# Optimization experiments

Hardware: AMD Instinct MI355X
Metric: run time of the kernel (lower is better)

The kernel has to match this reference:

```python
import jax, jax.numpy as jnp
import numpy as np

H = 16      # num_heads
D = 64      # hidden_size per head
IN = 1024   # input_size = H*D
B, S = 4, 2048

def setup_inputs() -> dict:
    key = jax.random.key(0)
    ks = jax.random.split(key, 5)
    scale = 1.0 / np.sqrt(IN)
    return {
        "x": jax.random.normal(ks[0], (B, S, IN), dtype=jnp.float32),
        "Wq": jax.random.normal(ks[1], (IN, H * D), dtype=jnp.float32) * scale,
        "bq": jnp.zeros((H * D,), dtype=jnp.float32),
        "Wk": jax.random.normal(ks[2], (IN, H * D), dtype=jnp.float32) * scale,
        "bk": jnp.zeros((H * D,), dtype=jnp.float32),
        "Wv": jax.random.normal(ks[3], (IN, H * D), dtype=jnp.float32) * scale,
        "bv": jnp.zeros((H * D,), dtype=jnp.float32),
        "Wo": jax.random.normal(ks[4], (H * D, IN), dtype=jnp.float32) * scale,
        "bo": jnp.zeros((IN,), dtype=jnp.float32),
    }

def reference(x, Wq, bq, Wk, bk, Wv, bv, Wo, bo):
    b, s, _ = x.shape
    # projections -> [b, h, s, d]
    def split_heads(t):
        return t.reshape(b, s, H, D).transpose(0, 2, 1, 3)
    q = split_heads(x @ Wq + bq)
    k = split_heads(x @ Wk + bk)
    v = split_heads(x @ Wv + bv)
    scores = jnp.einsum('bhqd,bhkd->bhqk', q, k) / jnp.sqrt(jnp.float32(D))
    probs = jax.nn.softmax(scores, axis=-1)            # [b,h,s,s]
    attn = jnp.einsum('bhqk,bhkd->bhqd', probs, v)     # [b,h,s,d]
    attn = attn.transpose(0, 2, 1, 3).reshape(b, s, H * D)
    out = attn @ Wo + bo
    return out, jnp.mean(probs, axis=1)
```

## Files before the change

### kernel.cpp

```cpp
#include <hip/hip_runtime.h>

typedef __attribute__((ext_vector_type(8))) short s8v;
typedef __attribute__((ext_vector_type(4))) short s4v;
typedef __attribute__((ext_vector_type(4))) float f4v;

#define DEV __device__ __forceinline__

DEV short b16(float f) {
  unsigned u = __builtin_bit_cast(unsigned, f);
  u = (u + 0x7fffu + ((u >> 16) & 1u)) >> 16;
  return (short)u;
}

DEV unsigned pk2(float a, float b) {
#if __has_builtin(__builtin_amdgcn_cvt_pk_bf16_f32)
  auto p = __builtin_amdgcn_cvt_pk_bf16_f32(a, b);
  return __builtin_bit_cast(unsigned, p);
#else
  return (unsigned)(unsigned short)b16(a) | ((unsigned)(unsigned short)b16(b) << 16);
#endif
}

DEV float fexp2(float x) {
#if __has_builtin(__builtin_amdgcn_exp2f)
  return __builtin_amdgcn_exp2f(x);
#else
  return exp2f(x);
#endif
}

DEV void gl_lds16(const short* g, short* l) {
  __builtin_amdgcn_global_load_lds((const __attribute__((address_space(1))) void*)g,
                                   (__attribute__((address_space(3))) void*)l, 16, 0, 0);
}

__global__ __launch_bounds__(256) void cast_f32_bf16(const float* __restrict__ in,
                                                     short* __restrict__ out, int n4) {
  int i = blockIdx.x * 256 + threadIdx.x;
  if (i >= n4) return;
  float4 v = ((const float4*)in)[i];
  s4v o; o.x = b16(v.x); o.y = b16(v.y); o.z = b16(v.z); o.w = b16(v.w);
  ((s4v*)out)[i] = o;
}

__global__ __launch_bounds__(256) void wtrans(const float* __restrict__ W, short* __restrict__ Wt) {
  int id = blockIdx.x * 256 + threadIdx.x;
  int k8 = id >> 10;
  int n  = id & 1023;
  s8v o;
#pragma unroll
  for (int j = 0; j < 8; ++j) o[j] = b16(W[(k8 * 8 + j) * 1024 + n]);
  *(s8v*)&Wt[n * 1024 + k8 * 8] = o;
}

template <bool OUT_BF16>
__global__ __launch_bounds__(256) void gemm128(const short* __restrict__ A,
                                               const short* __restrict__ Bt,
                                               const float* __restrict__ bias,
                                               void* __restrict__ Cout, float scale) {
  __shared__ short As[128 * 64];
  __shared__ short Bs[128 * 64];
  const int tid = threadIdx.x;
  const int w = tid >> 6, lane = tid & 63, quad = lane >> 4, l15 = lane & 15;
  const int wm = w >> 1, wn = w & 1;
  const int m0 = blockIdx.y * 128, n0 = blockIdx.x * 128;
  const int lr = lane >> 3, lc = (lane & 7) * 8;
  f4v acc[4][4] = {};
  for (int k0 = 0; k0 < 1024; k0 += 64) {
#pragma unroll
    for (int i = 0; i < 4; ++i) {
      int c = i * 4 + w;
      int r = c * 8 + lr;
      gl_lds16(&A[(m0 + r) * 1024 + k0 + lc], &As[c * 512]);
      gl_lds16(&Bt[(n0 + r) * 1024 + k0 + lc], &Bs[c * 512]);
    }
    __syncthreads();
#pragma unroll
    for (int kk = 0; kk < 2; ++kk) {
      s8v af[4], bf[4];
#pragma unroll
      for (int mt = 0; mt < 4; ++mt) af[mt] = *(const s8v*)&As[(wm * 64 + mt * 16 + l15) * 64 + kk * 32 + quad * 8];
#pragma unroll
      for (int nt = 0; nt < 4; ++nt) bf[nt] = *(const s8v*)&Bs[(wn * 64 + nt * 16 + l15) * 64 + kk * 32 + quad * 8];
#pragma unroll
      for (int mt = 0; mt < 4; ++mt)
#pragma unroll
        for (int nt = 0; nt < 4; ++nt)
          acc[mt][nt] = __builtin_amdgcn_mfma_f32_16x16x32_bf16(af[mt], bf[nt], acc[mt][nt], 0, 0, 0);
    }
    __syncthreads();
  }
#pragma unroll
  for (int nt = 0; nt < 4; ++nt) {
    const int col = n0 + wn * 64 + nt * 16 + l15;
    const float bcol = bias[col];
#pragma unroll
    for (int mt = 0; mt < 4; ++mt)
#pragma unroll
      for (int r = 0; r < 4; ++r) {
        const int row = m0 + wm * 64 + mt * 16 + quad * 4 + r;
        float v = (acc[mt][nt][r] + bcol) * scale;
        if (OUT_BF16) ((short*)Cout)[row * 1024 + col] = b16(v);
        else          ((float*)Cout)[row * 1024 + col] = v;
      }
  }
}

__global__ __launch_bounds__(256) void vtrans(const short* __restrict__ V, short* __restrict__ Vt) {
  __shared__ short T[128][72];
  const int st = blockIdx.x, h = blockIdx.y, b = blockIdx.z;
  const int tid = threadIdx.x;
#pragma unroll
  for (int i = 0; i < 4; ++i) {
    int c = tid + i * 256;
    int r = c >> 3, c8 = (c & 7) * 8;
    *(s8v*)&T[r][c8] = *(const s8v*)&V[((b * 2048 + st * 128 + r) * 16 + h) * 64 + c8];
  }
  __syncthreads();
#pragma unroll
  for (int i = 0; i < 4; ++i) {
    int id = tid + i * 256;
    int d = id & 63, s8 = id >> 6;
    s8v o;
#pragma unroll
    for (int j = 0; j < 8; ++j) o[j] = T[s8 * 8 + j][d];
    *(s8v*)&Vt[((b * 16 + h) * 64 + d) * 2048 + st * 128 + s8 * 8] = o;
  }
}

__global__ __launch_bounds__(256, 3) void attn_ctx(const short* __restrict__ Q, const short* __restrict__ K,
                                                   const short* __restrict__ Vt,
                                                   float* __restrict__ rbuf, short* __restrict__ ctx) {
  __shared__ __align__(16) char smem[50432];
  short* Ks = (short*)smem;
  short* Vs = (short*)(smem + 16384);
  short* Ps = (short*)(smem + 32768);
  short* Qs = Ps;
  float* l_part = (float*)(smem + 49152);
  float* l_s    = (float*)(smem + 50176);
  const int q64 = blockIdx.x, h = blockIdx.y, b = blockIdx.z;
  const int tid = threadIdx.x, w = tid >> 6, lane = tid & 63, quad = lane >> 4, l15 = lane & 15;
  const int bh = b * 16 + h, q0 = q64 * 64;

#pragma unroll
  for (int i = 0; i < 2; ++i) {
    int c = tid + i * 256;
    int r = c >> 3, cc = c & 7;
    *(s8v*)&Qs[r * 64 + (((cc ^ (r & 7))) << 3)] =
        *(const s8v*)&Q[((b * 2048 + q0 + r) * 16 + h) * 64 + cc * 8];
  }
  __syncthreads();
  s8v qf[4][2];
#pragma unroll
  for (int nt = 0; nt < 4; ++nt) {
    int r = nt * 16 + l15;
    qf[nt][0] = *(const s8v*)&Qs[r * 64 + ((quad ^ (r & 7)) << 3)];
    qf[nt][1] = *(const s8v*)&Qs[r * 64 + (((4 + quad) ^ (r & 7)) << 3)];
  }
  const short* kbase = &K[((long)(b * 2048) * 16 + h) * 64];
  const short* vbase = &Vt[(long)(bh * 64) * 2048];
  const int krow = w * 8 + (lane >> 3);
  const short* ksrc = kbase + krow * 1024 + (((lane & 7) ^ (lane >> 3)) << 3);
  const int vrow = w * 4 + (lane >> 4);
  const short* vsrc = vbase + vrow * 2048 + (((lane & 15) ^ vrow) << 3);
  f4v o[4] = {};
  float l_acc[4] = {0.f, 0.f, 0.f, 0.f};

  for (int kt = 0; kt < 16; ++kt) {
    __syncthreads();
#pragma unroll
    for (int i = 0; i < 4; ++i) {
      gl_lds16(ksrc + kt * 131072 + i * 32768, &Ks[(i * 4 + w) * 512]);
      gl_lds16(vsrc + kt * 128 + i * 32768, &Vs[(i * 4 + w) * 512]);
    }
    __syncthreads();
#pragma unroll
    for (int mt = 0; mt < 2; ++mt) {
      int kr = w * 32 + mt * 16 + l15;
      s8v a0 = *(const s8v*)&Ks[kr * 64 + ((quad ^ (kr & 7)) << 3)];
      s8v a1 = *(const s8v*)&Ks[kr * 64 + (((4 + quad) ^ (kr & 7)) << 3)];
#pragma unroll
      for (int nt = 0; nt < 4; ++nt) {
        f4v st = {};
        st = __builtin_amdgcn_mfma_f32_16x16x32_bf16(a0, qf[nt][0], st, 0, 0, 0);
        st = __builtin_amdgcn_mfma_f32_16x16x32_bf16(a1, qf[nt][1], st, 0, 0, 0);
        float e0 = fexp2(st[0]), e1 = fexp2(st[1]);
        float e2 = fexp2(st[2]), e3 = fexp2(st[3]);
        l_acc[nt] += (e0 + e1) + (e2 + e3);
        uint2 pp; pp.x = pk2(e0, e1); pp.y = pk2(e2, e3);
        int q = nt * 16 + l15;
        int chunk = (w * 4 + mt * 2 + (quad >> 1)) ^ l15;
        *(uint2*)&Ps[q * 128 + (chunk << 3) + (quad & 1) * 4] = pp;
      }
    }
    __syncthreads();
#pragma unroll
    for (int kk = 0; kk < 4; ++kk) {
      int qr = w * 16 + l15;
      s8v a = *(const s8v*)&Ps[qr * 128 + (((kk * 4 + quad) ^ (qr & 15)) << 3)];
#pragma unroll
      for (int dt = 0; dt < 4; ++dt) {
        int d = dt * 16 + l15;
        s8v vb = *(const s8v*)&Vs[d * 128 + (((kk * 4 + quad) ^ (d & 15)) << 3)];
        o[dt] = __builtin_amdgcn_mfma_f32_16x16x32_bf16(a, vb, o[dt], 0, 0, 0);
      }
    }
  }

#pragma unroll
  for (int nt = 0; nt < 4; ++nt) {
    float v = l_acc[nt];
    v += __shfl_xor(v, 16, 64);
    v += __shfl_xor(v, 32, 64);
    if (quad == 0) l_part[w * 64 + nt * 16 + l15] = v;
  }
  __syncthreads();
  if (tid < 64) {
    float s = l_part[tid] + l_part[64 + tid] + l_part[128 + tid] + l_part[192 + tid];
    float rv = 1.0f / s;
    l_s[tid] = rv;
    rbuf[bh * 2048 + q0 + tid] = rv;
  }
  __syncthreads();
  float rvq[4];
#pragma unroll
  for (int r = 0; r < 4; ++r) rvq[r] = l_s[w * 16 + quad * 4 + r];
#pragma unroll
  for (int dt = 0; dt < 4; ++dt)
#pragma unroll
    for (int r = 0; r < 4; ++r) {
      int sq = q0 + w * 16 + quad * 4 + r;
      ctx[((b * 2048 + sq) * 16 + h) * 64 + dt * 16 + l15] = b16(o[dt][r] * rvq[r]);
    }
}

__global__ __launch_bounds__(256) void mean_probs(const short* __restrict__ Q, const short* __restrict__ K,
                                                  const float* __restrict__ rbuf, float* __restrict__ outm) {
  __shared__ __align__(16) short Qs[8192];
  __shared__ __align__(16) short Ks[8192];
  __shared__ float r_s[128];
  const int k128 = blockIdx.x, q128 = blockIdx.y, b = blockIdx.z;
  const int tid = threadIdx.x, w = tid >> 6, lane = tid & 63, quad = lane >> 4, l15 = lane & 15;
  f4v mn[2][8] = {};
  const int mrow = w * 8 + (lane >> 3);
  const int mck8 = ((lane & 7) ^ (lane >> 3)) << 3;
  const short* qsrc = Q + ((long)(b * 2048 + q128 * 128 + mrow) * 16) * 64 + mck8;
  const short* ksrc = K + ((long)(b * 2048 + k128 * 128 + mrow) * 16) * 64 + mck8;
  for (int h = 0; h < 16; ++h) {
    __syncthreads();
#pragma unroll
    for (int i = 0; i < 4; ++i) {
      gl_lds16(qsrc + h * 64 + i * 32768, &Qs[(i * 4 + w) * 512]);
      gl_lds16(ksrc + h * 64 + i * 32768, &Ks[(i * 4 + w) * 512]);
    }
    if (tid < 128) r_s[tid] = rbuf[(b * 16 + h) * 2048 + q128 * 128 + tid] * 0.0625f;
    __syncthreads();
    s8v aq[2][2];
#pragma unroll
    for (int qt = 0; qt < 2; ++qt) {
      int r = w * 32 + qt * 16 + l15;
      aq[qt][0] = *(const s8v*)&Qs[r * 64 + ((quad ^ (r & 7)) << 3)];
      aq[qt][1] = *(const s8v*)&Qs[r * 64 + (((4 + quad) ^ (r & 7)) << 3)];
    }
    float rr[2][4];
#pragma unroll
    for (int qt = 0; qt < 2; ++qt)
#pragma unroll
      for (int r = 0; r < 4; ++r) rr[qt][r] = r_s[w * 32 + qt * 16 + quad * 4 + r];
#pragma unroll
    for (int ktile = 0; ktile < 8; ++ktile) {
      int kr = ktile * 16 + l15;
      s8v b0 = *(const s8v*)&Ks[kr * 64 + ((quad ^ (kr & 7)) << 3)];
      s8v b1 = *(const s8v*)&Ks[kr * 64 + (((4 + quad) ^ (kr & 7)) << 3)];
#pragma unroll
      for (int qt = 0; qt < 2; ++qt) {
        f4v sc = {};
        sc = __builtin_amdgcn_mfma_f32_16x16x32_bf16(aq[qt][0], b0, sc, 0, 0, 0);
        sc = __builtin_amdgcn_mfma_f32_16x16x32_bf16(aq[qt][1], b1, sc, 0, 0, 0);
#pragma unroll
        for (int r = 0; r < 4; ++r)
          mn[qt][ktile][r] += fexp2(sc[r]) * rr[qt][r];
      }
    }
  }
#pragma unroll
  for (int qt = 0; qt < 2; ++qt)
#pragma unroll
    for (int ktile = 0; ktile < 8; ++ktile)
#pragma unroll
      for (int r = 0; r < 4; ++r) {
        long qrow = q128 * 128 + w * 32 + qt * 16 + quad * 4 + r;
        outm[((long)b * 2048 + qrow) * 2048 + k128 * 128 + ktile * 16 + l15] = mn[qt][ktile][r];
      }
}

extern "C" void kernel_launch(void* const* d_in, const int* in_sizes, int n_in,
                              void* d_out, int out_size, void* d_ws, size_t ws_size,
                              hipStream_t stream) {
  (void)in_sizes; (void)n_in; (void)out_size; (void)ws_size;
  const float* x  = (const float*)d_in[0];
  const float* Wq = (const float*)d_in[1];
  const float* bq = (const float*)d_in[2];
  const float* Wk = (const float*)d_in[3];
  const float* bk = (const float*)d_in[4];
  const float* Wv = (const float*)d_in[5];
  const float* bv = (const float*)d_in[6];
  const float* Wo = (const float*)d_in[7];
  const float* bo = (const float*)d_in[8];
  float* out  = (float*)d_out;
  float* outm = out + 8388608;

  char* ws = (char*)d_ws;
  short* xb  = (short*)(ws);
  short* Wqt = (short*)(ws + 16777216);
  short* Wkt = (short*)(ws + 18874368);
  short* Wvt = (short*)(ws + 20971520);
  short* Wot = (short*)(ws + 23068672);
  short* Qb  = (short*)(ws + 25165824);
  short* Kb  = (short*)(ws + 41943040);
  short* Vb  = (short*)(ws + 58720256);
  short* Vt  = (short*)(ws + 75497472);
  float* rbuf = (float*)Vb;
  short* ctx = xb;

  const float C2 = 0.18033688011112042f;

  cast_f32_bf16<<<8192, 256, 0, stream>>>(x, xb, 2097152);
  wtrans<<<512, 256, 0, stream>>>(Wq, Wqt);
  wtrans<<<512, 256, 0, stream>>>(Wk, Wkt);
  wtrans<<<512, 256, 0, stream>>>(Wv, Wvt);
  wtrans<<<512, 256, 0, stream>>>(Wo, Wot);
  dim3 gg(8, 64);
  gemm128<true><<<gg, 256, 0, stream>>>(xb, Wqt, bq, Qb, C2);
  gemm128<true><<<gg, 256, 0, stream>>>(xb, Wkt, bk, Kb, 1.0f);
  gemm128<true><<<gg, 256, 0, stream>>>(xb, Wvt, bv, Vb, 1.0f);
  vtrans<<<dim3(16, 16, 4), 256, 0, stream>>>(Vb, Vt);
  attn_ctx<<<dim3(32, 16, 4), 256, 0, stream>>>(Qb, Kb, Vt, rbuf, ctx);
  mean_probs<<<dim3(16, 16, 4), 256, 0, stream>>>(Qb, Kb, rbuf, outm);
  gemm128<false><<<gg, 256, 0, stream>>>(ctx, Wot, bo, out, 1.0f);
}
```

Baseline: 445.4 us.

## Software-pipeline K/V and Q/K loads in attention and mean-probs kernels

The attention kernel now issues the next tile's K loads during the PV phase and the next V loads after it, with manual vmcnt waits and barriers in place of full __syncthreads. The mean_probs kernel double-buffers Q/K tiles in LDS, prefetches all reciprocal row sums up front, and moves the 1/16 scaling to the final store. The goal is to hide global-to-LDS latency behind MFMA work, at the cost of more LDS use and fragile hand-placed waitcnt ordering.

```diff
diff --git a/kernel.cpp b/kernel.cpp
--- a/kernel.cpp
+++ b/kernel.cpp
@@ -33,6 +33,10 @@
   __builtin_amdgcn_global_load_lds((const __attribute__((address_space(1))) void*)g,
                                    (__attribute__((address_space(3))) void*)l, 16, 0, 0);
 }
+
+#define WAIT_VM(N) asm volatile("s_waitcnt vmcnt(" #N ")" ::: "memory")
+#define WAIT_LGKM0() asm volatile("s_waitcnt lgkmcnt(0)" ::: "memory")
+#define BAR() __builtin_amdgcn_s_barrier()
 
 __global__ __launch_bounds__(256) void cast_f32_bf16(const float* __restrict__ in,
                                                      short* __restrict__ out, int n4) {
@@ -166,14 +170,15 @@
   f4v o[4] = {};
   float l_acc[4] = {0.f, 0.f, 0.f, 0.f};
 
+#pragma unroll
+  for (int i = 0; i < 4; ++i) gl_lds16(ksrc + i * 32768, &Ks[(i * 4 + w) * 512]);
+#pragma unroll
+  for (int i = 0; i < 4; ++i) gl_lds16(vsrc + i * 32768, &Vs[(i * 4 + w) * 512]);
+  WAIT_LGKM0();
+
   for (int kt = 0; kt < 16; ++kt) {
-    __syncthreads();
-#pragma unroll
-    for (int i = 0; i < 4; ++i) {
-      gl_lds16(ksrc + kt * 131072 + i * 32768, &Ks[(i * 4 + w) * 512]);
-      gl_lds16(vsrc + kt * 128 + i * 32768, &Vs[(i * 4 + w) * 512]);
-    }
-    __syncthreads();
+    WAIT_VM(4);
+    BAR();
 #pragma unroll
     for (int mt = 0; mt < 2; ++mt) {
       int kr = w * 32 + mt * 16 + l15;
@@ -193,7 +198,16 @@
         *(uint2*)&Ps[q * 128 + (chunk << 3) + (quad & 1) * 4] = pp;
       }
     }
-    __syncthreads();
+    WAIT_LGKM0();
+    BAR();
+    if (kt < 15) {
+#pragma unroll
+      for (int i = 0; i < 4; ++i) gl_lds16(ksrc + (kt + 1) * 131072 + i * 32768, &Ks[(i * 4 + w) * 512]);
+      WAIT_VM(4);
+    } else {
+      WAIT_VM(0);
+    }
+    BAR();
 #pragma unroll
     for (int kk = 0; kk < 4; ++kk) {
       int qr = w * 16 + l15;
@@ -204,6 +218,12 @@
         s8v vb = *(const s8v*)&Vs[d * 128 + (((kk * 4 + quad) ^ (d & 15)) << 3)];
         o[dt] = __builtin_amdgcn_mfma_f32_16x16x32_bf16(a, vb, o[dt], 0, 0, 0);
       }
+    }
+    WAIT_LGKM0();
+    BAR();
+    if (kt < 15) {
+#pragma unroll
+      for (int i = 0; i < 4; ++i) gl_lds16(vsrc + (kt + 1) * 128 + i * 32768, &Vs[(i * 4 + w) * 512]);
     }
   }
 
@@ -236,9 +256,9 @@
 
 __global__ __launch_bounds__(256) void mean_probs(const short* __restrict__ Q, const short* __restrict__ K,
                                                   const float* __restrict__ rbuf, float* __restrict__ outm) {
-  __shared__ __align__(16) short Qs[8192];
-  __shared__ __align__(16) short Ks[8192];
-  __shared__ float r_s[128];
+  __shared__ __align__(16) short Qs[2][8192];
+  __shared__ __align__(16) short Ks[2][8192];
+  __shared__ __align__(16) float r_all[2048];
   const int k128 = blockIdx.x, q128 = blockIdx.y, b = blockIdx.z;
   const int tid = threadIdx.x, w = tid >> 6, lane = tid & 63, quad = lane >> 4, l15 = lane & 15;
   f4v mn[2][8] = {};
@@ -246,32 +266,46 @@
   const int mck8 = ((lane & 7) ^ (lane >> 3)) << 3;
   const short* qsrc = Q + ((long)(b * 2048 + q128 * 128 + mrow) * 16) * 64 + mck8;
   const short* ksrc = K + ((long)(b * 2048 + k128 * 128 + mrow) * 16) * 64 + mck8;
+  const float* rb = rbuf + (long)(b * 16) * 2048 + q128 * 128;
+#pragma unroll
+  for (int i = 0; i < 2; ++i) {
+    int hh = i * 8 + w * 2 + (lane >> 5);
+    gl_lds16((const short*)(rb + hh * 2048 + (lane & 31) * 4), (short*)r_all + (i * 4 + w) * 512);
+  }
+#pragma unroll
+  for (int i = 0; i < 4; ++i) gl_lds16(qsrc + i * 32768, &Qs[0][(i * 4 + w) * 512]);
+#pragma unroll
+  for (int i = 0; i < 4; ++i) gl_lds16(ksrc + i * 32768, &Ks[0][(i * 4 + w) * 512]);
+
   for (int h = 0; h < 16; ++h) {
-    __syncthreads();
-#pragma unroll
-    for (int i = 0; i < 4; ++i) {
-      gl_lds16(qsrc + h * 64 + i * 32768, &Qs[(i * 4 + w) * 512]);
-      gl_lds16(ksrc + h * 64 + i * 32768, &Ks[(i * 4 + w) * 512]);
-    }
-    if (tid < 128) r_s[tid] = rbuf[(b * 16 + h) * 2048 + q128 * 128 + tid] * 0.0625f;
-    __syncthreads();
+    const int cur = h & 1;
+    if (h < 15) {
+#pragma unroll
+      for (int i = 0; i < 4; ++i) gl_lds16(qsrc + (h + 1) * 64 + i * 32768, &Qs[cur ^ 1][(i * 4 + w) * 512]);
+#pragma unroll
+      for (int i = 0; i < 4; ++i) gl_lds16(ksrc + (h + 1) * 64 + i * 32768, &Ks[cur ^ 1][(i * 4 + w) * 512]);
+      WAIT_VM(8);
+    } else {
+      WAIT_VM(0);
+    }
+    BAR();
     s8v aq[2][2];
 #pragma unroll
     for (int qt = 0; qt < 2; ++qt) {
       int r = w * 32 + qt * 16 + l15;
-      aq[qt][0] = *(const s8v*)&Qs[r * 64 + ((quad ^ (r & 7)) << 3)];
-      aq[qt][1] = *(const s8v*)&Qs[r * 64 + (((4 + quad) ^ (r & 7)) << 3)];
+      aq[qt][0] = *(const s8v*)&Qs[cur][r * 64 + ((quad ^ (r & 7)) << 3)];
+      aq[qt][1] = *(const s8v*)&Qs[cur][r * 64 + (((4 + quad) ^ (r & 7)) << 3)];
     }
     float rr[2][4];
 #pragma unroll
     for (int qt = 0; qt < 2; ++qt)
 #pragma unroll
-      for (int r = 0; r < 4; ++r) rr[qt][r] = r_s[w * 32 + qt * 16 + quad * 4 + r];
+      for (int r = 0; r < 4; ++r) rr[qt][r] = r_all[h * 128 + w * 32 + qt * 16 + quad * 4 + r];
 #pragma unroll
     for (int ktile = 0; ktile < 8; ++ktile) {
       int kr = ktile * 16 + l15;
-      s8v b0 = *(const s8v*)&Ks[kr * 64 + ((quad ^ (kr & 7)) << 3)];
-      s8v b1 = *(const s8v*)&Ks[kr * 64 + (((4 + quad) ^ (kr & 7)) << 3)];
+      s8v b0 = *(const s8v*)&Ks[cur][kr * 64 + ((quad ^ (kr & 7)) << 3)];
+      s8v b1 = *(const s8v*)&Ks[cur][kr * 64 + (((4 + quad) ^ (kr & 7)) << 3)];
 #pragma unroll
       for (int qt = 0; qt < 2; ++qt) {
         f4v sc = {};
@@ -282,6 +316,8 @@
           mn[qt][ktile][r] += fexp2(sc[r]) * rr[qt][r];
       }
     }
+    WAIT_LGKM0();
+    BAR();
   }
 #pragma unroll
   for (int qt = 0; qt < 2; ++qt)
@@ -290,7 +326,7 @@
 #pragma unroll
       for (int r = 0; r < 4; ++r) {
         long qrow = q128 * 128 + w * 32 + qt * 16 + quad * 4 + r;
-        outm[((long)b * 2048 + qrow) * 2048 + k128 * 128 + ktile * 16 + l15] = mn[qt][ktile][r];
+        outm[((long)b * 2048 + qrow) * 2048 + k128 * 128 + ktile * 16 + l15] = mn[qt][ktile][r] * 0.0625f;
       }
 }
 
```

After: 438.8 us. About the same (-1.5%).
